# Kernel optimization log

Measured on AMD Instinct MI355X. Metric: run time of the kernel, lower is better.

The kernel has to match this reference:

```python
import jax, jax.numpy as jnp
import numpy as np

N, D, K = 32768, 256, 2048
BETA = 0.25  # init arg beta, in [0,1) branch of the loss


def setup_inputs() -> dict:
    key = jax.random.key(0)
    k1, k2 = jax.random.split(key)
    x = jax.random.normal(k1, (N, D), dtype=jnp.float32)
    # mimics nn.Embedding init: uniform(-1/K, 1/K) then mean-centered
    cb = jax.random.uniform(k2, (K, D), dtype=jnp.float32, minval=-1.0 / K, maxval=1.0 / K)
    codebook = cb - cb.mean(axis=0)
    return {"x": x, "codebook": codebook}


def reference(x, codebook):
    # pairwise squared L2 distances: [N, K]
    dist = (
        jnp.sum(x * x, axis=1, keepdims=True)
        + jnp.sum(codebook * codebook, axis=1)
        - 2.0 * jnp.matmul(x, codebook.T)
    )
    encoding_inds = jnp.argmin(dist, axis=1)  # [N]
    # one-hot @ codebook == gather of nearest code vectors
    x_codebook = jnp.take(codebook, encoding_inds, axis=0)  # [N, D]
    # straight-through quantization
    x_quantized = x + jax.lax.stop_gradient(x_codebook - x)
    # VQ loss, beta in [0, 1) branch
    commit = jnp.mean((x - jax.lax.stop_gradient(x_codebook)) ** 2)
    embed = jnp.mean((x_codebook - jax.lax.stop_gradient(x)) ** 2)
    loss = BETA * commit + embed
    return x_quantized, loss
```

## Files before the change

### kernel.cpp

```cpp
#include <hip/hip_runtime.h>

#define N_ROWS 32768
#define DIM    256
#define KCODES 2048
#define CSCALE 4096.0f
#define BROWS  64

typedef __attribute__((ext_vector_type(16))) float f32x16;
typedef __attribute__((ext_vector_type(8)))  int   i32x8;
typedef __attribute__((ext_vector_type(4)))  unsigned int u32x4;

union frag32 { i32x8 v8; u32x4 q[2]; };

__device__ __forceinline__ uint4 pack16(const float* s) {
    int a = __builtin_amdgcn_cvt_pk_fp8_f32(s[0],  s[1],  0, false);
    a     = __builtin_amdgcn_cvt_pk_fp8_f32(s[2],  s[3],  a, true);
    int b = __builtin_amdgcn_cvt_pk_fp8_f32(s[4],  s[5],  0, false);
    b     = __builtin_amdgcn_cvt_pk_fp8_f32(s[6],  s[7],  b, true);
    int c = __builtin_amdgcn_cvt_pk_fp8_f32(s[8],  s[9],  0, false);
    c     = __builtin_amdgcn_cvt_pk_fp8_f32(s[10], s[11], c, true);
    int d = __builtin_amdgcn_cvt_pk_fp8_f32(s[12], s[13], 0, false);
    d     = __builtin_amdgcn_cvt_pk_fp8_f32(s[14], s[15], d, true);
    uint4 o; o.x = a; o.y = b; o.z = c; o.w = d;
    return o;
}

__global__ void prep_h(const float* __restrict__ cb,
                       float* __restrict__ halfcn, float* __restrict__ loss) {
    const int t    = threadIdx.x;
    const int code = blockIdx.x * 4 + (t >> 6);
    const int s    = t & 63;
    if (blockIdx.x == 0 && t == 0) *loss = 0.0f;
    const int k0 = s * 4;
    float4 v = *(const float4*)&cb[(size_t)code * DIM + k0];
    float ssum = v.x * v.x + v.y * v.y + v.z * v.z + v.w * v.w;
    #pragma unroll
    for (int o = 32; o > 0; o >>= 1) ssum += __shfl_down(ssum, o, 64);
    if (s == 0) halfcn[code] = 0.5f * CSCALE * ssum;
}

__global__ void prep_frag(const float* __restrict__ cb, uint4* __restrict__ cbF) {
    const int gid  = blockIdx.x * 256 + threadIdx.x;
    const int tile = gid >> 9;
    const int r9   = gid & 511;
    const int c    = r9 >> 7;
    const int r7   = r9 & 127;
    const int u    = r7 >> 6;
    const int L    = r7 & 63;
    const int l32  = L & 31, h = L >> 5;
    const int code = tile * 32 + l32;
    const int k0   = c * 64 + h * 32 + u * 16;
    float buf[16];
    #pragma unroll
    for (int b = 0; b < 4; b++) {
        float4 v = *(const float4*)&cb[(size_t)code * DIM + k0 + b * 4];
        buf[b * 4 + 0] = v.x * CSCALE; buf[b * 4 + 1] = v.y * CSCALE;
        buf[b * 4 + 2] = v.z * CSCALE; buf[b * 4 + 3] = v.w * CSCALE;
    }
    cbF[gid] = pack16(buf);
}

__global__ __launch_bounds__(256, 2) void vq_fused(
        const float* __restrict__ x, const float* __restrict__ cb,
        const uint4* __restrict__ cbF, const float* __restrict__ halfcn,
        float* __restrict__ out, float* __restrict__ loss) {
    __shared__ char As[2][8192];
    __shared__ float hcs[KCODES];
    struct Tail { float red[BROWS][4]; int idxs[BROWS]; float lred[4]; };
    Tail* tl = (Tail*)As;

    const int t    = threadIdx.x;
    const int lane = t & 63;
    const int w    = t >> 6;
    const int l32  = lane & 31;
    const int h    = lane >> 5;
    const int row0 = blockIdx.x * BROWS;
    char* asb = &As[0][0];

    {
        const int r  = t >> 2;
        const int q4 = t & 3;
        const int rt = r >> 5, rw = r & 31;
        const float* src = x + (size_t)(row0 + r) * DIM;
        float buf[16];
        #pragma unroll
        for (int g = 0; g < 4; g++) {
            const int o16 = q4 * 4 + g;
            #pragma unroll
            for (int j = 0; j < 4; j++)
                *(float4*)(buf + j * 4) = *(const float4*)(src + o16 * 16 + j * 4);
            *(uint4*)(asb + rt * 8192 + rw * 256 + ((o16 ^ (rw & 7)) << 4)) = pack16(buf);
        }
        #pragma unroll
        for (int jj = 0; jj < 8; jj++) hcs[jj * 256 + t] = halfcn[jj * 256 + t];
    }

    float mp[2][16];
    #pragma unroll
    for (int rt = 0; rt < 2; rt++)
        #pragma unroll
        for (int r = 0; r < 16; r++) mp[rt][r] = -3.0e38f;

    const char* bbase = (const char*)cbF + (size_t)(w * 16) * 8192 + (size_t)lane * 16;

    frag32 bfr[2][4];
    #pragma unroll
    for (int s = 0; s < 2; s++)
        #pragma unroll
        for (int c = 0; c < 4; c++)
            #pragma unroll
            for (int u = 0; u < 2; u++)
                bfr[s][c].q[u] = *(const u32x4*)(bbase + s * 8192 + c * 2048 + u * 1024);

    __syncthreads();

    frag32 afr[4][2];
    #pragma unroll
    for (int c = 0; c < 4; c++)
        #pragma unroll
        for (int rt = 0; rt < 2; rt++)
            #pragma unroll
            for (int u = 0; u < 2; u++) {
                const int o16 = c * 4 + h * 2 + u;
                afr[c][rt].q[u] = *(const u32x4*)(
                    asb + rt * 8192 + l32 * 256 + ((o16 ^ (l32 & 7)) << 4));
            }

    #pragma unroll
    for (int tt = 0; tt < 16; ++tt) {
        const int sl = tt & 1;
        const float hc = hcs[(w * 16 + tt) * 32 + l32];
        f32x16 acc[2];
        #pragma unroll
        for (int r = 0; r < 16; r++) { acc[0][r] = -hc; acc[1][r] = -hc; }

        #pragma unroll
        for (int c = 0; c < 4; c++)
            #pragma unroll
            for (int rt = 0; rt < 2; rt++)
                acc[rt] = __builtin_amdgcn_mfma_scale_f32_32x32x64_f8f6f4(
                    afr[c][rt].v8, bfr[sl][c].v8, acc[rt],
                    0, 0,
                    0, 127,
                    0, 127);

        if (tt + 2 < 16) {
            #pragma unroll
            for (int c = 0; c < 4; c++)
                #pragma unroll
                for (int u = 0; u < 2; u++)
                    bfr[sl][c].q[u] = *(const u32x4*)(
                        bbase + (tt + 2) * 8192 + c * 2048 + u * 1024);
        }

        const unsigned code = (unsigned)((w * 16 + tt) * 32 + l32);
        #pragma unroll
        for (int rt = 0; rt < 2; rt++)
            #pragma unroll
            for (int r = 0; r < 16; r++) {
                unsigned u = (__float_as_uint(acc[rt][r]) & 0xFFFFF800u) | code;
                mp[rt][r] = fmaxf(mp[rt][r], __uint_as_float(u));
            }
    }

    #pragma unroll
    for (int m = 1; m <= 16; m <<= 1)
        #pragma unroll
        for (int rt = 0; rt < 2; rt++)
            #pragma unroll
            for (int r = 0; r < 16; r++)
                mp[rt][r] = fmaxf(mp[rt][r], __shfl_xor(mp[rt][r], m, 64));

    __syncthreads();

    if (l32 == 0) {
        #pragma unroll
        for (int rt = 0; rt < 2; rt++)
            #pragma unroll
            for (int r = 0; r < 16; r++) {
                const int row = rt * 32 + (r & 3) + 8 * (r >> 2) + 4 * h;
                tl->red[row][w] = mp[rt][r];
            }
    }
    __syncthreads();
    if (t < BROWS) {
        float b0 = fmaxf(fmaxf(tl->red[t][0], tl->red[t][1]),
                         fmaxf(tl->red[t][2], tl->red[t][3]));
        tl->idxs[t] = (int)(__float_as_uint(b0) & 2047u);
    }
    __syncthreads();

    float lsum = 0.0f;
    #pragma unroll 4
    for (int r = 0; r < BROWS; r++) {
        const int code = tl->idxs[r];
        const float c  = cb[(size_t)code * DIM + t];
        const float xv = x[(size_t)(row0 + r) * DIM + t];
        out[(size_t)(row0 + r) * DIM + t] = c;
        const float d = xv - c;
        lsum += d * d;
    }
    #pragma unroll
    for (int o = 32; o > 0; o >>= 1) lsum += __shfl_down(lsum, o, 64);
    if (lane == 0) tl->lred[w] = lsum;
    __syncthreads();
    if (t == 0) {
        const float scale = 1.25f / (float)((size_t)N_ROWS * DIM);
        atomicAdd(loss, (tl->lred[0] + tl->lred[1] + tl->lred[2] + tl->lred[3]) * scale);
    }
}

extern "C" void kernel_launch(void* const* d_in, const int* in_sizes, int n_in,
                              void* d_out, int out_size, void* d_ws, size_t ws_size,
                              hipStream_t stream) {
    const float* x  = (const float*)d_in[0];
    const float* cb = (const float*)d_in[1];
    float* out  = (float*)d_out;
    float* loss = out + (size_t)N_ROWS * DIM;

    char* ws = (char*)d_ws;
    uint4* cbF    = (uint4*)ws;
    float* halfcn = (float*)(ws + (size_t)KCODES * 256);

    prep_h   <<<KCODES / 4, 256, 0, stream>>>(cb, halfcn, loss);
    prep_frag<<<128,        256, 0, stream>>>(cb, cbF);
    vq_fused <<<N_ROWS / BROWS, 256, 0, stream>>>(x, cb, cbF, halfcn, out, loss);
}
```

Before: 123.7 us.

## Double-buffer MFMA accumulators, merge prep kernels, relax launch bounds

The main loop now keeps two accumulator sets, so the argmax fold of the previous tile runs after the MFMAs of the next tile are issued. This lets VALU work overlap with matrix-core work. The two preprocessing kernels are merged into one launch to save a kernel launch. Launch bounds drop from 2 blocks per CU to 1, which gives more registers for the extra accumulators but may lower occupancy and latency hiding.

```diff
diff --git a/kernel.cpp b/kernel.cpp
--- a/kernel.cpp
+++ b/kernel.cpp
@@ -25,42 +25,42 @@
     return o;
 }
 
-__global__ void prep_h(const float* __restrict__ cb,
-                       float* __restrict__ halfcn, float* __restrict__ loss) {
+__global__ void prep_all(const float* __restrict__ cb, uint4* __restrict__ cbF,
+                         float* __restrict__ halfcn, float* __restrict__ loss) {
     const int t    = threadIdx.x;
-    const int code = blockIdx.x * 4 + (t >> 6);
-    const int s    = t & 63;
     if (blockIdx.x == 0 && t == 0) *loss = 0.0f;
-    const int k0 = s * 4;
-    float4 v = *(const float4*)&cb[(size_t)code * DIM + k0];
-    float ssum = v.x * v.x + v.y * v.y + v.z * v.z + v.w * v.w;
-    #pragma unroll
-    for (int o = 32; o > 0; o >>= 1) ssum += __shfl_down(ssum, o, 64);
-    if (s == 0) halfcn[code] = 0.5f * CSCALE * ssum;
-}
-
-__global__ void prep_frag(const float* __restrict__ cb, uint4* __restrict__ cbF) {
-    const int gid  = blockIdx.x * 256 + threadIdx.x;
-    const int tile = gid >> 9;
-    const int r9   = gid & 511;
-    const int c    = r9 >> 7;
-    const int r7   = r9 & 127;
-    const int u    = r7 >> 6;
-    const int L    = r7 & 63;
-    const int l32  = L & 31, h = L >> 5;
-    const int code = tile * 32 + l32;
-    const int k0   = c * 64 + h * 32 + u * 16;
-    float buf[16];
-    #pragma unroll
-    for (int b = 0; b < 4; b++) {
-        float4 v = *(const float4*)&cb[(size_t)code * DIM + k0 + b * 4];
-        buf[b * 4 + 0] = v.x * CSCALE; buf[b * 4 + 1] = v.y * CSCALE;
-        buf[b * 4 + 2] = v.z * CSCALE; buf[b * 4 + 3] = v.w * CSCALE;
-    }
-    cbF[gid] = pack16(buf);
-}
-
-__global__ __launch_bounds__(256, 2) void vq_fused(
+    {
+        const int code = blockIdx.x * 4 + (t >> 6);
+        const int s    = t & 63;
+        float4 v = *(const float4*)&cb[(size_t)code * DIM + s * 4];
+        float ssum = v.x * v.x + v.y * v.y + v.z * v.z + v.w * v.w;
+        #pragma unroll
+        for (int o = 32; o > 0; o >>= 1) ssum += __shfl_down(ssum, o, 64);
+        if (s == 0) halfcn[code] = 0.5f * CSCALE * ssum;
+    }
+    if (blockIdx.x < 128) {
+        const int gid  = blockIdx.x * 256 + t;
+        const int tile = gid >> 9;
+        const int r9   = gid & 511;
+        const int c    = r9 >> 7;
+        const int r7   = r9 & 127;
+        const int u    = r7 >> 6;
+        const int L    = r7 & 63;
+        const int l32  = L & 31, h = L >> 5;
+        const int code = tile * 32 + l32;
+        const int k0   = c * 64 + h * 32 + u * 16;
+        float buf[16];
+        #pragma unroll
+        for (int b = 0; b < 4; b++) {
+            float4 v = *(const float4*)&cb[(size_t)code * DIM + k0 + b * 4];
+            buf[b * 4 + 0] = v.x * CSCALE; buf[b * 4 + 1] = v.y * CSCALE;
+            buf[b * 4 + 2] = v.z * CSCALE; buf[b * 4 + 3] = v.w * CSCALE;
+        }
+        cbF[gid] = pack16(buf);
+    }
+}
+
+__global__ __launch_bounds__(256, 1) void vq_fused(
         const float* __restrict__ x, const float* __restrict__ cb,
         const uint4* __restrict__ cbF, const float* __restrict__ halfcn,
         float* __restrict__ out, float* __restrict__ loss) {
@@ -126,33 +126,31 @@
                     asb + rt * 8192 + l32 * 256 + ((o16 ^ (l32 & 7)) << 4));
             }
 
-    #pragma unroll
-    for (int tt = 0; tt < 16; ++tt) {
-        const int sl = tt & 1;
+    f32x16 accA[2], accB[2];
+
+    auto initAcc = [&](f32x16* acc, int tt) {
         const float hc = hcs[(w * 16 + tt) * 32 + l32];
-        f32x16 acc[2];
         #pragma unroll
         for (int r = 0; r < 16; r++) { acc[0][r] = -hc; acc[1][r] = -hc; }
-
+    };
+    auto mfmaTile = [&](f32x16* acc, int sl) {
         #pragma unroll
         for (int c = 0; c < 4; c++)
             #pragma unroll
             for (int rt = 0; rt < 2; rt++)
                 acc[rt] = __builtin_amdgcn_mfma_scale_f32_32x32x64_f8f6f4(
                     afr[c][rt].v8, bfr[sl][c].v8, acc[rt],
-                    0, 0,
-                    0, 127,
-                    0, 127);
-
-        if (tt + 2 < 16) {
-            #pragma unroll
-            for (int c = 0; c < 4; c++)
-                #pragma unroll
-                for (int u = 0; u < 2; u++)
-                    bfr[sl][c].q[u] = *(const u32x4*)(
-                        bbase + (tt + 2) * 8192 + c * 2048 + u * 1024);
-        }
-
+                    0, 0, 0, 127, 0, 127);
+    };
+    auto refill = [&](int sl, int tile) {
+        #pragma unroll
+        for (int c = 0; c < 4; c++)
+            #pragma unroll
+            for (int u = 0; u < 2; u++)
+                bfr[sl][c].q[u] = *(const u32x4*)(
+                    bbase + tile * 8192 + c * 2048 + u * 1024);
+    };
+    auto fold = [&](const f32x16* acc, int tt) {
         const unsigned code = (unsigned)((w * 16 + tt) * 32 + l32);
         #pragma unroll
         for (int rt = 0; rt < 2; rt++)
@@ -161,7 +159,22 @@
                 unsigned u = (__float_as_uint(acc[rt][r]) & 0xFFFFF800u) | code;
                 mp[rt][r] = fmaxf(mp[rt][r], __uint_as_float(u));
             }
-    }
+    };
+
+    initAcc(accA, 0);
+    mfmaTile(accA, 0);
+    refill(0, 2);
+
+    #pragma unroll
+    for (int tt = 1; tt < 16; ++tt) {
+        const int sl = tt & 1;
+        if (tt & 1) { initAcc(accB, tt); mfmaTile(accB, sl); }
+        else        { initAcc(accA, tt); mfmaTile(accA, sl); }
+        if (tt + 2 < 16) refill(sl, tt + 2);
+        if (tt & 1) fold(accA, tt - 1);
+        else        fold(accB, tt - 1);
+    }
+    fold(accB, 15);
 
     #pragma unroll
     for (int m = 1; m <= 16; m <<= 1)
@@ -222,7 +235,6 @@
     uint4* cbF    = (uint4*)ws;
     float* halfcn = (float*)(ws + (size_t)KCODES * 256);
 
-    prep_h   <<<KCODES / 4, 256, 0, stream>>>(cb, halfcn, loss);
-    prep_frag<<<128,        256, 0, stream>>>(cb, cbF);
-    vq_fused <<<N_ROWS / BROWS, 256, 0, stream>>>(x, cb, cbF, halfcn, out, loss);
-}
+    prep_all<<<KCODES / 4, 256, 0, stream>>>(cb, cbF, halfcn, loss);
+    vq_fused<<<N_ROWS / BROWS, 256, 0, stream>>>(x, cb, cbF, halfcn, out, loss);
+}
```

Result: faster. 120.3 us (-2.7%).
